# Kernel optimization log

Hardware: AMD Instinct MI355X
Metric: run time of the kernel (lower is better)

## Reference

```python
import jax, jax.numpy as jnp
import numpy as np

N = 50000   # nodes
E = 800000  # edges (avg degree 16)
D = 128     # dim_node_features
G = 128     # num_graphs
NP = 25000  # post nodes
NI = 25000  # image nodes
L = 2       # num_gnn_layers
EPS = 1e-5


def setup_inputs() -> dict:
    key = jax.random.key(0)
    ks = jax.random.split(key, 24)
    f = lambda k, shp, s: jax.random.normal(k, shp, jnp.float32) * s
    inp = {
        "x": f(ks[0], (N, D), 1.0),
        "W_gnn": f(ks[1], (L, D, D), D ** -0.5),
        "b_gnn": f(ks[2], (L, D), 0.02),
        "hbn_gamma": 1.0 + f(ks[3], (D,), 0.02),
        "hbn_beta": f(ks[4], (D,), 0.02),
        "gf_w1": f(ks[5], (4 * D, D), (4 * D) ** -0.5),
        "gf_b1": f(ks[6], (D,), 0.02),
        "gf_w2": f(ks[7], (D, D), D ** -0.5),
        "gf_b2": f(ks[8], (D,), 0.02),
        "bn2_gamma": 1.0 + f(ks[9], (D,), 0.02),
        "bn2_beta": f(ks[10], (D,), 0.02),
        "fl_w1": f(ks[11], (D, 64), D ** -0.5),
        "fl_b1": f(ks[12], (64,), 0.02),
        "fl_w2": f(ks[13], (64, 32), 64 ** -0.5),
        "fl_b2": f(ks[14], (32,), 0.02),
        "out_w": f(ks[15], (32, 2), 32 ** -0.5),
        "out_b": f(ks[16], (2,), 0.02),
        "edge_index": jax.random.randint(ks[17], (2, E), 0, N, jnp.int32),
        "post_idx": jax.random.randint(ks[18], (NP,), 0, N, jnp.int32),
        "image_idx": jax.random.randint(ks[19], (NI,), 0, N, jnp.int32),
        "batch_vec": jnp.sort(jax.random.randint(ks[20], (N,), 0, G, jnp.int32)),
    }
    return inp


def _bn(x, gamma, beta):
    # BatchNorm1d, training mode: biased batch statistics
    m = jnp.mean(x, axis=0)
    v = jnp.var(x, axis=0)
    return (x - m) * jax.lax.rsqrt(v + EPS) * gamma + beta


def _mean_pool(feat, seg):
    s = jax.ops.segment_sum(feat, seg, num_segments=G)
    c = jax.ops.segment_sum(jnp.ones(seg.shape[0], feat.dtype), seg, num_segments=G)
    return s / jnp.clip(c, 1.0)[:, None]


def reference(x, W_gnn, b_gnn, hbn_gamma, hbn_beta, gf_w1, gf_b1, gf_w2, gf_b2,
              bn2_gamma, bn2_beta, fl_w1, fl_b1, fl_w2, fl_b2, out_w, out_b,
              edge_index, post_idx, image_idx, batch_vec):
    src, dst = edge_index[0], edge_index[1]
    # GCN symmetric normalization with self loops: deg includes the self loop
    deg = jax.ops.segment_sum(jnp.ones(E, x.dtype), dst, num_segments=N) + 1.0
    dis = deg ** -0.5  # deg^-1/2
    enorm = (dis[src] * dis[dst])[:, None]   # per-edge norm
    snorm = (dis * dis)[:, None]             # self-loop norm
    H = x
    for i in range(L):
        xw = H @ W_gnn[i]                                   # [N, D]
        agg = jax.ops.segment_sum(xw[src] * enorm, dst, num_segments=N)
        H = agg + xw * snorm + b_gnn[i]
        H = jax.nn.leaky_relu(H)
    H = _bn(H, hbn_gamma, hbn_beta)
    pf = _mean_pool(H[post_idx], batch_vec[post_idx])        # [G, D]
    imf = _mean_pool(H[image_idx], batch_vec[image_idx])     # [G, D]
    comb = jnp.concatenate([pf, imf, pf - imf, pf * imf], axis=-1)  # [G, 4D]
    # generate_feature (dropout = identity, eval)
    h = jax.nn.leaky_relu(comb @ gf_w1 + gf_b1) @ gf_w2 + gf_b2
    h = _bn(h, bn2_gamma, bn2_beta)
    # feature_layer (encodeMLP)
    out = jax.nn.leaky_relu(h @ fl_w1 + fl_b1) @ fl_w2 + fl_b2  # [G, 32]
    prob = out @ out_w + out_b                                   # [G, 2]
    return out, prob
```

## Files before the change

### kernel.cpp

```cpp
#include <hip/hip_runtime.h>
#include <hip/hip_bf16.h>
#include <math.h>

#define DF 128
#define PSPLIT 4
#define CHUNK 8192
#define NBK 256
#define CAP 6144
#define LEAKY(x) ((x) > 0.f ? (x) : 0.01f * (x))

typedef __attribute__((ext_vector_type(8))) short short8v;
typedef __attribute__((ext_vector_type(4))) float f32x4;
typedef __attribute__((ext_vector_type(4))) unsigned short u16x4;
typedef __attribute__((ext_vector_type(8))) unsigned short u16x8;

static __device__ __forceinline__ unsigned short f2bf(float f) {
  unsigned u = __float_as_uint(f);
  unsigned r = u + 0x7fffu + ((u >> 16) & 1u);
  return (unsigned short)(r >> 16);
}
static __device__ __forceinline__ float bf2f(unsigned short b) {
  return __uint_as_float(((unsigned)b) << 16);
}

__global__ void fusedA_k(const int* __restrict__ post_idx, const int* __restrict__ image_idx,
                         const int* __restrict__ batch, int* __restrict__ pcnt,
                         int* __restrict__ icnt,
                         const float* __restrict__ W, unsigned short* __restrict__ Wb,
                         int NP, int NI, int wTotal, int PB) {
  int b = blockIdx.x;
  if (b < PB) {
    int i = b * 256 + threadIdx.x;
    if (i < NP) atomicAdd(&pcnt[batch[post_idx[i]]], 1);
    else if (i < NP + NI) atomicAdd(&icnt[batch[image_idx[i - NP]]], 1);
  } else {
    int i = (b - PB) * 256 + threadIdx.x;
    if (i < wTotal) {
      int layer = i >> 14, o = i & 16383;
      int j = o & 7, l = (o >> 3) & 63, ks = (o >> 9) & 3, ct = (o >> 11) & 3, wc = (o >> 13) & 1;
      int row = ks * 32 + (l >> 4) * 8 + j;
      int col = wc * 64 + ct * 16 + (l & 15);
      Wb[i] = f2bf(W[((size_t)layer << 14) + row * DF + col]);
    }
  }
}

__global__ void __launch_bounds__(256) bucket_fill_k(const int* __restrict__ src,
                                                     const int* __restrict__ dst,
                                                     int* __restrict__ bcur,
                                                     int* __restrict__ ebuck, int nE) {
  __shared__ int hist[NBK];
  __shared__ int base[NBK];
  __shared__ int gbase[NBK];
  __shared__ int lpack[CHUNK];
  __shared__ unsigned char lbk[CHUNK];
  int e0 = blockIdx.x * CHUNK;
  int cnt = nE - e0; if (cnt > CHUNK) cnt = CHUNK;
  hist[threadIdx.x] = 0;
  __syncthreads();
  for (int i = threadIdx.x; i < cnt; i += 256)
    atomicAdd(&hist[dst[e0 + i] >> 8], 1);
  __syncthreads();
  int t = threadIdx.x;
  base[t] = hist[t];
  __syncthreads();
  for (int ofs = 1; ofs < NBK; ofs <<= 1) {
    int tv = (t >= ofs) ? base[t - ofs] : 0;
    __syncthreads();
    base[t] += tv;
    __syncthreads();
  }
  int excl = base[t] - hist[t];
  __syncthreads();
  base[t] = excl;
  hist[t] = 0;
  __syncthreads();
  for (int i = threadIdx.x; i < cnt; i += 256) {
    int d = dst[e0 + i], s = src[e0 + i];
    int bk = d >> 8;
    int pos = base[bk] + atomicAdd(&hist[bk], 1);
    lpack[pos] = (s << 8) | (d & 255);
    lbk[pos] = (unsigned char)bk;
  }
  __syncthreads();
  int c = hist[t];
  gbase[t] = c > 0 ? (t * CAP + atomicAdd(&bcur[t], c)) : 0;
  __syncthreads();
  for (int i = threadIdx.x; i < cnt; i += 256) {
    int bk = lbk[i];
    ebuck[gbase[bk] + (i - base[bk])] = lpack[i];
  }
}

__global__ void __launch_bounds__(1024) scan3_k(
    const int* __restrict__ bcur, int* __restrict__ boff2, int NBUCK,
    const int* __restrict__ pcnt, int* __restrict__ poff, int* __restrict__ pcur,
    const int* __restrict__ icnt, int* __restrict__ ioff, int* __restrict__ icur, int G) {
  const int* in; int* out; int* cur; int n;
  if (blockIdx.x == 0)      { in = bcur; out = boff2; cur = nullptr; n = NBUCK; }
  else if (blockIdx.x == 1) { in = pcnt; out = poff;  cur = pcur;    n = G; }
  else                      { in = icnt; out = ioff;  cur = icur;    n = G; }
  __shared__ int sh[1024];
  int v = (threadIdx.x < (unsigned)n) ? in[threadIdx.x] : 0;
  sh[threadIdx.x] = v;
  __syncthreads();
  for (int ofs = 1; ofs < 1024; ofs <<= 1) {
    int t = (threadIdx.x >= (unsigned)ofs) ? sh[threadIdx.x - ofs] : 0;
    __syncthreads();
    sh[threadIdx.x] += t;
    __syncthreads();
  }
  if (threadIdx.x < (unsigned)n) {
    int ex = sh[threadIdx.x] - v;
    out[threadIdx.x] = ex;
    if (cur) cur[threadIdx.x] = ex;
  }
  if (threadIdx.x == 0) out[n] = sh[1023];
}

__global__ void __launch_bounds__(256) csr_build_k(const int* __restrict__ bcnt,
                                                   const int* __restrict__ boff2,
                                                   const int* __restrict__ ebuck,
                                                   int* __restrict__ rowoff,
                                                   float* __restrict__ dis,
                                                   int2* __restrict__ epack,
                                                   int N, int NBUCK) {
  int b = blockIdx.x;
  int cnt = bcnt[b];
  int ob = boff2[b];
  const int* ebk = ebuck + (size_t)b * CAP;
  int node0 = b << 8;
  __shared__ int hist[NBK];
  __shared__ int lbase[NBK];
  int t = threadIdx.x;
  hist[t] = 0;
  __syncthreads();
  for (int i = t; i < cnt; i += 256)
    atomicAdd(&hist[ebk[i] & 255], 1);
  __syncthreads();
  int v = hist[t];
  lbase[t] = v;
  __syncthreads();
  for (int ofs = 1; ofs < NBK; ofs <<= 1) {
    int tv = (t >= ofs) ? lbase[t - ofs] : 0;
    __syncthreads();
    lbase[t] += tv;
    __syncthreads();
  }
  int excl = lbase[t] - v;
  __syncthreads();
  lbase[t] = excl;
  hist[t] = 0;
  int node = node0 + t;
  if (node < N) {
    rowoff[node] = ob + excl;
    dis[node] = 1.0f / sqrtf((float)v + 1.0f);
  }
  if (b == NBUCK - 1 && t == 0) rowoff[N] = ob + cnt;
  __syncthreads();
  for (int i = t; i < cnt; i += 256) {
    int e = ebk[i];
    int loc = e & 255;
    int pos = ob + lbase[loc] + atomicAdd(&hist[loc], 1);
    int2 w; w.x = e >> 8; w.y = node0 + loc;
    epack[pos] = w;
  }
}

template<bool BF16A>
static __device__ __forceinline__ void gemm_body(int bid, int tid,
                                                 const float* __restrict__ A,
                                                 const unsigned short* __restrict__ Ab,
                                                 const unsigned short* __restrict__ Wb,
                                                 unsigned short* __restrict__ xwb, int n) {
  const int w = tid >> 6, l = tid & 63;
  const int wr = w & 1, wc = w >> 1;
  const int r0 = bid * 32 + wr * 16;
  const int row = r0 + (l & 15);
  const int kg = l >> 4;
  short8v bf[4][4];
  const unsigned short* wp = Wb + (size_t)wc * 8192 + (size_t)l * 8;
#pragma unroll
  for (int ct = 0; ct < 4; ++ct)
#pragma unroll
    for (int ks = 0; ks < 4; ++ks)
      bf[ct][ks] = *(const short8v*)(wp + ((ct * 4 + ks) << 9));
  const bool rok = row < n;
  short8v af[4];
  if constexpr (BF16A) {
    const unsigned short* ap = Ab + (size_t)row * DF + kg * 8;
#pragma unroll
    for (int ks = 0; ks < 4; ++ks)
      af[ks] = rok ? *(const short8v*)(ap + ks * 32) : (short8v)0;
  } else {
    const float* ap = A + (size_t)row * DF + kg * 8;
#pragma unroll
    for (int ks = 0; ks < 4; ++ks) {
      if (rok) {
        float4 lo = *(const float4*)(ap + ks * 32);
        float4 hi = *(const float4*)(ap + ks * 32 + 4);
        short8v t;
        t[0] = (short)f2bf(lo.x); t[1] = (short)f2bf(lo.y);
        t[2] = (short)f2bf(lo.z); t[3] = (short)f2bf(lo.w);
        t[4] = (short)f2bf(hi.x); t[5] = (short)f2bf(hi.y);
        t[6] = (short)f2bf(hi.z); t[7] = (short)f2bf(hi.w);
        af[ks] = t;
      } else af[ks] = (short8v)0;
    }
  }
  f32x4 acc[4];
#pragma unroll
  for (int ct = 0; ct < 4; ++ct) acc[ct] = (f32x4)(0.f);
#pragma unroll
  for (int ks = 0; ks < 4; ++ks)
#pragma unroll
    for (int ct = 0; ct < 4; ++ct)
      acc[ct] = __builtin_amdgcn_mfma_f32_16x16x32_bf16(af[ks], bf[ct][ks], acc[ct], 0, 0, 0);
#pragma unroll
  for (int ct = 0; ct < 4; ++ct) {
    int c = wc * 64 + ct * 16 + (l & 15);
#pragma unroll
    for (int rg = 0; rg < 4; ++rg) {
      int r = r0 + kg * 4 + rg;
      if (r < n) xwb[(size_t)r * DF + c] = f2bf(acc[ct][rg]);
    }
  }
}

__global__ void __launch_bounds__(256) gemm_mfma_k(const unsigned short* __restrict__ Ab,
                                                   const unsigned short* __restrict__ Wb,
                                                   unsigned short* __restrict__ xwb, int n) {
  gemm_body<true>(blockIdx.x, threadIdx.x, nullptr, Ab, Wb, xwb, n);
}

__global__ void __launch_bounds__(256) fusedB_k(const float* __restrict__ x,
                        const unsigned short* __restrict__ Wb, unsigned short* __restrict__ xwb,
                        int2* __restrict__ epack, const float* __restrict__ dis, int E,
                        const int* __restrict__ post_idx, const int* __restrict__ image_idx,
                        const int* __restrict__ batch, int* __restrict__ pcur,
                        int* __restrict__ icur, int* __restrict__ plist,
                        int* __restrict__ ilist, int NP, int NI,
                        int n, int GB, int EN) {
  int b = blockIdx.x;
  if (b < GB) {
    gemm_body<false>(b, threadIdx.x, x, nullptr, Wb, xwb, n);
  } else if (b < GB + EN) {
    int i = (b - GB) * 256 + threadIdx.x;
    if (i < E) {
      int2 w = epack[i];
      epack[i].y = __float_as_int(dis[w.x] * dis[w.y]);
    }
  } else {
    int i = (b - GB - EN) * 256 + threadIdx.x;
    if (i < NP) {
      int nd = post_idx[i];
      int p = atomicAdd(&pcur[batch[nd]], 1);
      plist[p] = nd;
    } else if (i < NP + NI) {
      int nd = image_idx[i - NP];
      int p = atomicAdd(&icur[batch[nd]], 1);
      ilist[p] = nd;
    }
  }
}

__global__ void gather_k(const unsigned short* __restrict__ xwb, const int* __restrict__ rowoff,
                         const int2* __restrict__ epack, const float* __restrict__ dis,
                         const float* __restrict__ b, unsigned short* __restrict__ Hb, int n) {
  int gid = blockIdx.x * 256 + threadIdx.x;
  int node = gid >> 5;
  if (node >= n) return;
  int part = gid & 15;
  int team = (gid >> 4) & 1;
  int beg = rowoff[node], end = rowoff[node + 1];
  float acc[8];
#pragma unroll
  for (int j = 0; j < 8; ++j) acc[j] = 0.f;
  int p = beg + team;
  for (; p + 14 < end; p += 16) {
    int2 q[8];
#pragma unroll
    for (int u = 0; u < 8; ++u) q[u] = epack[p + 2 * u];
    u16x8 v[8];
#pragma unroll
    for (int u = 0; u < 8; ++u) v[u] = *(const u16x8*)(xwb + (size_t)q[u].x * DF + part * 8);
#pragma unroll
    for (int u = 0; u < 8; ++u) {
      float e = __int_as_float(q[u].y);
#pragma unroll
      for (int j = 0; j < 8; ++j) acc[j] = fmaf(bf2f(v[u][j]), e, acc[j]);
    }
  }
  for (; p + 6 < end; p += 8) {
    int2 q0 = epack[p], q1 = epack[p + 2], q2 = epack[p + 4], q3 = epack[p + 6];
    float e0 = __int_as_float(q0.y), e1 = __int_as_float(q1.y);
    float e2 = __int_as_float(q2.y), e3 = __int_as_float(q3.y);
    u16x8 v0 = *(const u16x8*)(xwb + (size_t)q0.x * DF + part * 8);
    u16x8 v1 = *(const u16x8*)(xwb + (size_t)q1.x * DF + part * 8);
    u16x8 v2 = *(const u16x8*)(xwb + (size_t)q2.x * DF + part * 8);
    u16x8 v3 = *(const u16x8*)(xwb + (size_t)q3.x * DF + part * 8);
#pragma unroll
    for (int j = 0; j < 8; ++j) {
      acc[j] = fmaf(bf2f(v0[j]), e0, acc[j]);
      acc[j] = fmaf(bf2f(v1[j]), e1, acc[j]);
      acc[j] = fmaf(bf2f(v2[j]), e2, acc[j]);
      acc[j] = fmaf(bf2f(v3[j]), e3, acc[j]);
    }
  }
  for (; p < end; p += 2) {
    int2 q = epack[p];
    float e = __int_as_float(q.y);
    u16x8 v = *(const u16x8*)(xwb + (size_t)q.x * DF + part * 8);
#pragma unroll
    for (int j = 0; j < 8; ++j) acc[j] = fmaf(bf2f(v[j]), e, acc[j]);
  }
#pragma unroll
  for (int j = 0; j < 8; ++j) acc[j] += __shfl_down(acc[j], 16, 32);
  if (team == 0) {
    float dd = dis[node], sn = dd * dd;
    u16x8 xv = *(const u16x8*)(xwb + (size_t)node * DF + part * 8);
    const float* bp = b + part * 8;
    u16x8 o;
#pragma unroll
    for (int j = 0; j < 8; ++j) {
      float r = fmaf(bf2f(xv[j]), sn, acc[j]) + bp[j];
      r = LEAKY(r);
      o[j] = f2bf(r);
    }
    *(u16x8*)(Hb + (size_t)node * DF + part * 8) = o;
  }
}

__global__ void post_k(const unsigned short* __restrict__ Hb,
                       const int* __restrict__ goff_p, const int* __restrict__ mlist_p,
                       const int* __restrict__ goff_i, const int* __restrict__ mlist_i,
                       float* __restrict__ psum, float* __restrict__ isum,
                       float* __restrict__ bns, int n, int PGB, int SB) {
  int b = blockIdx.x;
  if (b < 2 * PGB) {
    int which = b >= PGB;
    int bb = which ? b - PGB : b;
    const int* goff  = which ? goff_i  : goff_p;
    const int* mlist = which ? mlist_i : mlist_p;
    float* out       = which ? isum    : psum;
    int g = bb / PSPLIT, sub = bb % PSPLIT;
    int part = threadIdx.x & 31, slot = threadIdx.x >> 5;
    int beg = goff[g], end = goff[g + 1];
    float4 acc = make_float4(0.f, 0.f, 0.f, 0.f);
    for (int j = beg + sub * 8 + slot; j < end; j += PSPLIT * 8) {
      u16x4 v = *(const u16x4*)(Hb + (size_t)mlist[j] * DF + part * 4);
      acc.x += bf2f(v[0]); acc.y += bf2f(v[1]); acc.z += bf2f(v[2]); acc.w += bf2f(v[3]);
    }
    __shared__ float4 sh[256];
    sh[threadIdx.x] = acc;
    __syncthreads();
    for (int ofs = 128; ofs >= 32; ofs >>= 1) {
      if (threadIdx.x < (unsigned)ofs) {
        float4 o = sh[threadIdx.x + ofs];
        float4 a = sh[threadIdx.x];
        a.x += o.x; a.y += o.y; a.z += o.z; a.w += o.w;
        sh[threadIdx.x] = a;
      }
      __syncthreads();
    }
    if (threadIdx.x < 32) {
      float4 a = sh[threadIdx.x];
      float* o = out + (size_t)g * DF + part * 4;
      atomicAdd(o + 0, a.x);
      atomicAdd(o + 1, a.y);
      atomicAdd(o + 2, a.z);
      atomicAdd(o + 3, a.w);
    }
  } else {
    int sb = b - 2 * PGB;
    int c = threadIdx.x & (DF - 1);
    int half = threadIdx.x >> 7;
    float s = 0.f, q = 0.f;
    for (int r = sb * 2 + half; r < n; r += SB * 2) {
      float v = bf2f(Hb[(size_t)r * DF + c]);
      s += v; q += v * v;
    }
    __shared__ float ls[256], lq[256];
    ls[threadIdx.x] = s; lq[threadIdx.x] = q;
    __syncthreads();
    if (half == 0) {
      atomicAdd(&bns[c], ls[c] + ls[c + DF]);
      atomicAdd(&bns[DF + c], lq[c] + lq[c + DF]);
    }
  }
}

__global__ void __launch_bounds__(512) head1_k(const float* __restrict__ psum,
                        const int* __restrict__ pcnt,
                        const float* __restrict__ isum, const int* __restrict__ icnt,
                        const float* __restrict__ bns, const float* __restrict__ hbn_gamma,
                        const float* __restrict__ hbn_beta, int nN,
                        const float* __restrict__ gf_w1, const float* __restrict__ gf_b1,
                        const float* __restrict__ gf_w2, const float* __restrict__ gf_b2,
                        float* __restrict__ hbuf) {
  int g = blockIdx.x;
  int j = threadIdx.x & 127, kq = threadIdx.x >> 7;
  __shared__ float comb[4 * DF];
  __shared__ float part[512];
  __shared__ float t1[DF];
  if (kq == 0) {
    float m = bns[j] / (float)nN;
    float var = bns[DF + j] / (float)nN - m * m;
    if (var < 0.f) var = 0.f;
    float sc = hbn_gamma[j] / sqrtf(var + 1e-5f);
    float sh = hbn_beta[j] - m * sc;
    int pc = pcnt[g], ic = icnt[g];
    float pf = pc > 0 ? (psum[(size_t)g * DF + j] / (float)pc) * sc + sh : 0.f;
    float im = ic > 0 ? (isum[(size_t)g * DF + j] / (float)ic) * sc + sh : 0.f;
    comb[j] = pf;
    comb[DF + j] = im;
    comb[2 * DF + j] = pf - im;
    comb[3 * DF + j] = pf * im;
  }
  __syncthreads();
  float acc = 0.f;
  const float* w1 = gf_w1 + (size_t)kq * 128 * DF + j;
#pragma unroll 8
  for (int kk = 0; kk < 128; ++kk)
    acc = fmaf(comb[kq * 128 + kk], w1[(size_t)kk * DF], acc);
  part[threadIdx.x] = acc;
  __syncthreads();
  if (kq == 0)
    t1[j] = LEAKY(gf_b1[j] + part[j] + part[128 + j] + part[256 + j] + part[384 + j]);
  __syncthreads();
  acc = 0.f;
  const float* w2 = gf_w2 + (size_t)kq * 32 * DF + j;
#pragma unroll 8
  for (int kk = 0; kk < 32; ++kk)
    acc = fmaf(t1[kq * 32 + kk], w2[(size_t)kk * DF], acc);
  part[threadIdx.x] = acc;
  __syncthreads();
  if (kq == 0)
    hbuf[(size_t)g * DF + j] = gf_b2[j] + part[j] + part[128 + j] + part[256 + j] + part[384 + j];
}

__global__ void __launch_bounds__(1024) bn2_k(const float* __restrict__ hbuf,
                      const float* __restrict__ gamma, const float* __restrict__ beta,
                      float* __restrict__ ss2, int G) {
  int c = threadIdx.x & 127, slot = threadIdx.x >> 7;
  float s = 0.f, q = 0.f;
  for (int r = slot; r < G; r += 8) {
    float v = hbuf[(size_t)r * DF + c];
    s += v; q += v * v;
  }
  __shared__ float ls[1024], lq[1024];
  ls[threadIdx.x] = s; lq[threadIdx.x] = q;
  __syncthreads();
  for (int ofs = 512; ofs >= 128; ofs >>= 1) {
    if (threadIdx.x < (unsigned)ofs) {
      ls[threadIdx.x] += ls[threadIdx.x + ofs];
      lq[threadIdx.x] += lq[threadIdx.x + ofs];
    }
    __syncthreads();
  }
  if (threadIdx.x < 128) {
    float m = ls[c] / (float)G;
    float var = lq[c] / (float)G - m * m;
    if (var < 0.f) var = 0.f;
    float sc = gamma[c] / sqrtf(var + 1e-5f);
    ss2[c] = sc;
    ss2[DF + c] = beta[c] - m * sc;
  }
}

__global__ void __launch_bounds__(512) head2_k(const float* __restrict__ hbuf,
                        const float* __restrict__ ss2,
                        const float* __restrict__ fl_w1, const float* __restrict__ fl_b1,
                        const float* __restrict__ fl_w2, const float* __restrict__ fl_b2,
                        const float* __restrict__ out_w, const float* __restrict__ out_b,
                        float* __restrict__ d_out, int G) {
  int g = blockIdx.x, t = threadIdx.x;
  __shared__ float hb[DF], part[512], t1[64], ov[32];
  if (t < DF) hb[t] = hbuf[(size_t)g * DF + t] * ss2[t] + ss2[DF + t];
  __syncthreads();
  {
    int j = t & 63, kq = t >> 6;
    float acc = 0.f;
    const float* w = fl_w1 + (size_t)kq * 16 * 64 + j;
#pragma unroll
    for (int kk = 0; kk < 16; ++kk)
      acc = fmaf(hb[kq * 16 + kk], w[(size_t)kk * 64], acc);
    part[t] = acc;
  }
  __syncthreads();
  if (t < 64) {
    float s = fl_b1[t];
#pragma unroll
    for (int i = 0; i < 8; ++i) s += part[i * 64 + t];
    t1[t] = LEAKY(s);
  }
  __syncthreads();
  {
    int j = t & 31, kq = t >> 5;
    float acc = 0.f;
    const float* w = fl_w2 + (size_t)kq * 4 * 32 + j;
#pragma unroll
    for (int kk = 0; kk < 4; ++kk)
      acc = fmaf(t1[kq * 4 + kk], w[(size_t)kk * 32], acc);
    part[t] = acc;
  }
  __syncthreads();
  if (t < 32) {
    float s = fl_b2[t];
#pragma unroll
    for (int i = 0; i < 16; ++i) s += part[i * 32 + t];
    d_out[(size_t)g * 32 + t] = s;
    ov[t] = s;
  }
  __syncthreads();
  if (t < 64) {
    int j = t & 1, kq = t >> 1;
    part[t] = ov[kq] * out_w[(size_t)kq * 2 + j];
  }
  __syncthreads();
  if (t < 2) {
    float s = out_b[t];
#pragma unroll
    for (int i = 0; i < 32; ++i) s += part[i * 2 + t];
    d_out[(size_t)G * 32 + (size_t)g * 2 + t] = s;
  }
}

extern "C" void kernel_launch(void* const* d_in, const int* in_sizes, int n_in,
                              void* d_out, int out_size, void* d_ws, size_t ws_size,
                              hipStream_t stream) {
  const float* x         = (const float*)d_in[0];
  const float* W_gnn     = (const float*)d_in[1];
  const float* b_gnn     = (const float*)d_in[2];
  const float* hbn_gamma = (const float*)d_in[3];
  const float* hbn_beta  = (const float*)d_in[4];
  const float* gf_w1     = (const float*)d_in[5];
  const float* gf_b1     = (const float*)d_in[6];
  const float* gf_w2     = (const float*)d_in[7];
  const float* gf_b2     = (const float*)d_in[8];
  const float* bn2_gamma = (const float*)d_in[9];
  const float* bn2_beta  = (const float*)d_in[10];
  const float* fl_w1     = (const float*)d_in[11];
  const float* fl_b1     = (const float*)d_in[12];
  const float* fl_w2     = (const float*)d_in[13];
  const float* fl_b2     = (const float*)d_in[14];
  const float* out_w     = (const float*)d_in[15];
  const float* out_b     = (const float*)d_in[16];
  const int* edge_index  = (const int*)d_in[17];
  const int* post_idx    = (const int*)d_in[18];
  const int* image_idx   = (const int*)d_in[19];
  const int* batch_vec   = (const int*)d_in[20];

  const int N  = in_sizes[20];
  const int E  = in_sizes[17] / 2;
  const int NP = in_sizes[18];
  const int NI = in_sizes[19];
  const int G  = out_size / 34;
  const int L  = in_sizes[1] / (DF * DF);
  const int* src  = edge_index;
  const int* dstp = edge_index + E;
  const int NBUCK = (N + 255) >> 8;
  const int PB = (NP + NI + 255) / 256;
  const int WT = L * DF * DF;
  const int WB = (WT + 255) / 256;
  const int GB = (N + 31) / 32;
  const int EN = (E + 255) / 256;
  const int PGB = G * PSPLIT;
  const int SB = 256;

  char* ws = (char*)d_ws;
  size_t off = 0;
  auto alloc = [&](size_t b) { size_t o = off; off += (b + 255) & ~(size_t)255; return o; };
  size_t zero_beg = off;
  int*   bcur   = (int*)(ws + alloc((size_t)NBK * 4));
  float* bns    = (float*)(ws + alloc(256 * 4));
  float* psum   = (float*)(ws + alloc((size_t)G * DF * 4));
  float* isum   = (float*)(ws + alloc((size_t)G * DF * 4));
  int*   pcnt   = (int*)(ws + alloc((size_t)G * 4));
  int*   icnt   = (int*)(ws + alloc((size_t)G * 4));
  size_t zero_bytes = off - zero_beg;
  float* dis    = (float*)(ws + alloc((size_t)N * 4));
  int*   rowoff = (int*)(ws + alloc((size_t)(N + 1) * 4));
  int2*  epack  = (int2*)(ws + alloc((size_t)E * 8));
  int*   ebuck  = (int*)(ws + alloc((size_t)NBUCK * CAP * 4));
  int*   boff2  = (int*)(ws + alloc((size_t)(NBK + 1) * 4));
  unsigned short* Wb  = (unsigned short*)(ws + alloc((size_t)WT * 2));
  unsigned short* xwb = (unsigned short*)(ws + alloc((size_t)N * DF * 2));
  unsigned short* Hb  = (unsigned short*)(ws + alloc((size_t)N * DF * 2));
  int*   poff   = (int*)(ws + alloc((size_t)(G + 1) * 4));
  int*   ioff   = (int*)(ws + alloc((size_t)(G + 1) * 4));
  int*   pcur   = (int*)(ws + alloc((size_t)G * 4));
  int*   icur   = (int*)(ws + alloc((size_t)G * 4));
  int*   plist  = (int*)(ws + alloc((size_t)NP * 4));
  int*   ilist  = (int*)(ws + alloc((size_t)NI * 4));
  float* hbuf   = (float*)(ws + alloc((size_t)G * DF * 4));
  float* ss2    = (float*)(ws + alloc(256 * 4));

  hipMemsetAsync(ws + zero_beg, 0, zero_bytes, stream);

  bucket_fill_k<<<(E + CHUNK - 1) / CHUNK, 256, 0, stream>>>(src, dstp, bcur, ebuck, E);
  fusedA_k<<<PB + WB, 256, 0, stream>>>(post_idx, image_idx, batch_vec, pcnt, icnt,
                                        W_gnn, Wb, NP, NI, WT, PB);
  scan3_k<<<3, 1024, 0, stream>>>(bcur, boff2, NBUCK, pcnt, poff, pcur, icnt, ioff, icur, G);
  csr_build_k<<<NBUCK, 256, 0, stream>>>(bcur, boff2, ebuck, rowoff, dis, epack, N, NBUCK);
  fusedB_k<<<GB + EN + PB, 256, 0, stream>>>(x, Wb, xwb, epack, dis, E,
                                             post_idx, image_idx, batch_vec,
                                             pcur, icur, plist, ilist, NP, NI, N, GB, EN);
  gather_k<<<(N * 32 + 255) / 256, 256, 0, stream>>>(xwb, rowoff, epack, dis,
                                                     b_gnn, Hb, N);
  for (int l = 1; l < L; ++l) {
    gemm_mfma_k<<<GB, 256, 0, stream>>>(Hb, Wb + (size_t)l * DF * DF, xwb, N);
    gather_k<<<(N * 32 + 255) / 256, 256, 0, stream>>>(xwb, rowoff, epack, dis,
                                                       b_gnn + (size_t)l * DF, Hb, N);
  }

  post_k<<<2 * PGB + SB, 256, 0, stream>>>(Hb, poff, plist, ioff, ilist,
                                           psum, isum, bns, N, PGB, SB);

  head1_k<<<G, 512, 0, stream>>>(psum, pcnt, isum, icnt, bns, hbn_gamma, hbn_beta, N,
                                 gf_w1, gf_b1, gf_w2, gf_b2, hbuf);
  bn2_k<<<1, 1024, 0, stream>>>(hbuf, bn2_gamma, bn2_beta, ss2, G);
  head2_k<<<G, 512, 0, stream>>>(hbuf, ss2, fl_w1, fl_b1, fl_w2, fl_b2, out_w, out_b,
                                 (float*)d_out, G);
}
```

Baseline: 248.2 us.

## Split fused GEMM/edge-norm kernel and drop 16-wide gather unroll

Un-fuses the first-layer GEMM from the edge-norm and pool-list kernel, so the GEMM launches as its own templated kernel and edge normalization plus pool bucketing run in a separate launch. It also removes the 8-edge-per-iteration unrolled loop in the gather kernel, leaving the 4-edge loop as the main path. This adds a kernel launch and may lose overlap between the GEMM and the edge work, but it shrinks register pressure and code size in the gather and in the heterogeneous fused kernel.

Result: faster. 232.7 us, median of 2 (-6.2%).

```diff
diff --git a/kernel.cpp b/kernel.cpp
--- a/kernel.cpp
+++ b/kernel.cpp
@@ -167,15 +167,40 @@
   }
 }
 
+__global__ void enormpool_k(int2* __restrict__ epack, const float* __restrict__ dis, int E,
+                            const int* __restrict__ post_idx, const int* __restrict__ image_idx,
+                            const int* __restrict__ batch, int* __restrict__ pcur,
+                            int* __restrict__ icur, int* __restrict__ plist,
+                            int* __restrict__ ilist, int NP, int NI, int EN) {
+  int b = blockIdx.x;
+  if (b < EN) {
+    int i = b * 256 + threadIdx.x;
+    if (i < E) {
+      int2 w = epack[i];
+      epack[i].y = __float_as_int(dis[w.x] * dis[w.y]);
+    }
+  } else {
+    int i = (b - EN) * 256 + threadIdx.x;
+    if (i < NP) {
+      int nd = post_idx[i];
+      int p = atomicAdd(&pcur[batch[nd]], 1);
+      plist[p] = nd;
+    } else if (i < NP + NI) {
+      int nd = image_idx[i - NP];
+      int p = atomicAdd(&icur[batch[nd]], 1);
+      ilist[p] = nd;
+    }
+  }
+}
+
 template<bool BF16A>
-static __device__ __forceinline__ void gemm_body(int bid, int tid,
-                                                 const float* __restrict__ A,
-                                                 const unsigned short* __restrict__ Ab,
-                                                 const unsigned short* __restrict__ Wb,
-                                                 unsigned short* __restrict__ xwb, int n) {
-  const int w = tid >> 6, l = tid & 63;
+__global__ void __launch_bounds__(256) gemm_mfma_k(const float* __restrict__ A,
+                                                   const unsigned short* __restrict__ Ab,
+                                                   const unsigned short* __restrict__ Wb,
+                                                   unsigned short* __restrict__ xwb, int n) {
+  const int w = threadIdx.x >> 6, l = threadIdx.x & 63;
   const int wr = w & 1, wc = w >> 1;
-  const int r0 = bid * 32 + wr * 16;
+  const int r0 = blockIdx.x * 32 + wr * 16;
   const int row = r0 + (l & 15);
   const int kg = l >> 4;
   short8v bf[4][4];
@@ -227,43 +252,6 @@
   }
 }
 
-__global__ void __launch_bounds__(256) gemm_mfma_k(const unsigned short* __restrict__ Ab,
-                                                   const unsigned short* __restrict__ Wb,
-                                                   unsigned short* __restrict__ xwb, int n) {
-  gemm_body<true>(blockIdx.x, threadIdx.x, nullptr, Ab, Wb, xwb, n);
-}
-
-__global__ void __launch_bounds__(256) fusedB_k(const float* __restrict__ x,
-                        const unsigned short* __restrict__ Wb, unsigned short* __restrict__ xwb,
-                        int2* __restrict__ epack, const float* __restrict__ dis, int E,
-                        const int* __restrict__ post_idx, const int* __restrict__ image_idx,
-                        const int* __restrict__ batch, int* __restrict__ pcur,
-                        int* __restrict__ icur, int* __restrict__ plist,
-                        int* __restrict__ ilist, int NP, int NI,
-                        int n, int GB, int EN) {
-  int b = blockIdx.x;
-  if (b < GB) {
-    gemm_body<false>(b, threadIdx.x, x, nullptr, Wb, xwb, n);
-  } else if (b < GB + EN) {
-    int i = (b - GB) * 256 + threadIdx.x;
-    if (i < E) {
-      int2 w = epack[i];
-      epack[i].y = __float_as_int(dis[w.x] * dis[w.y]);
-    }
-  } else {
-    int i = (b - GB - EN) * 256 + threadIdx.x;
-    if (i < NP) {
-      int nd = post_idx[i];
-      int p = atomicAdd(&pcur[batch[nd]], 1);
-      plist[p] = nd;
-    } else if (i < NP + NI) {
-      int nd = image_idx[i - NP];
-      int p = atomicAdd(&icur[batch[nd]], 1);
-      ilist[p] = nd;
-    }
-  }
-}
-
 __global__ void gather_k(const unsigned short* __restrict__ xwb, const int* __restrict__ rowoff,
                          const int2* __restrict__ epack, const float* __restrict__ dis,
                          const float* __restrict__ b, unsigned short* __restrict__ Hb, int n) {
@@ -277,20 +265,6 @@
 #pragma unroll
   for (int j = 0; j < 8; ++j) acc[j] = 0.f;
   int p = beg + team;
-  for (; p + 14 < end; p += 16) {
-    int2 q[8];
-#pragma unroll
-    for (int u = 0; u < 8; ++u) q[u] = epack[p + 2 * u];
-    u16x8 v[8];
-#pragma unroll
-    for (int u = 0; u < 8; ++u) v[u] = *(const u16x8*)(xwb + (size_t)q[u].x * DF + part * 8);
-#pragma unroll
-    for (int u = 0; u < 8; ++u) {
-      float e = __int_as_float(q[u].y);
-#pragma unroll
-      for (int j = 0; j < 8; ++j) acc[j] = fmaf(bf2f(v[u][j]), e, acc[j]);
-    }
-  }
   for (; p + 6 < end; p += 8) {
     int2 q0 = epack[p], q1 = epack[p + 2], q2 = epack[p + 4], q3 = epack[p + 6];
     float e0 = __int_as_float(q0.y), e1 = __int_as_float(q1.y);
@@ -603,13 +577,16 @@
                                         W_gnn, Wb, NP, NI, WT, PB);
   scan3_k<<<3, 1024, 0, stream>>>(bcur, boff2, NBUCK, pcnt, poff, pcur, icnt, ioff, icur, G);
   csr_build_k<<<NBUCK, 256, 0, stream>>>(bcur, boff2, ebuck, rowoff, dis, epack, N, NBUCK);
-  fusedB_k<<<GB + EN + PB, 256, 0, stream>>>(x, Wb, xwb, epack, dis, E,
-                                             post_idx, image_idx, batch_vec,
-                                             pcur, icur, plist, ilist, NP, NI, N, GB, EN);
-  gather_k<<<(N * 32 + 255) / 256, 256, 0, stream>>>(xwb, rowoff, epack, dis,
-                                                     b_gnn, Hb, N);
-  for (int l = 1; l < L; ++l) {
-    gemm_mfma_k<<<GB, 256, 0, stream>>>(Hb, Wb + (size_t)l * DF * DF, xwb, N);
+  enormpool_k<<<EN + PB, 256, 0, stream>>>(epack, dis, E, post_idx, image_idx, batch_vec,
+                                           pcur, icur, plist, ilist, NP, NI, EN);
+
+  for (int l = 0; l < L; ++l) {
+    if (l == 0)
+      gemm_mfma_k<false><<<GB, 256, 0, stream>>>(x, nullptr,
+          Wb + (size_t)l * DF * DF, xwb, N);
+    else
+      gemm_mfma_k<true><<<GB, 256, 0, stream>>>(nullptr, Hb,
+          Wb + (size_t)l * DF * DF, xwb, N);
     gather_k<<<(N * 32 + 255) / 256, 256, 0, stream>>>(xwb, rowoff, epack, dis,
                                                        b_gnn + (size_t)l * DF, Hb, N);
   }
```
